# Kernel optimization log

Measured on AMD Instinct MI355X. Metric: run time of the kernel, lower is better.

Reference implementation:

```python
import jax, jax.numpy as jnp
import numpy as np

B, S, HID = 1, 2048, 2048
NH, NKV = 16, 4
HD = HID // NH  # 128


def _rope_manual(x, cos_h, sin_h):
    # x: [B, S, nh, HD]; cos_h/sin_h: [1, S, 1, HD//2]
    d = x.shape[-1]
    x_rot = x[..., : d // 2]
    x_pass = x[..., d // 2:]
    # rotate interleaved pairs inside the first half
    x_rot = jnp.stack([-x_rot[..., 1::2], x_rot[..., ::2]], axis=-1)
    x_rot = x_rot.reshape(x_rot.shape[:-2] + (d // 2,))
    return jnp.concatenate(
        [x_rot * cos_h + x_pass * sin_h, -x_rot * sin_h + x_pass * cos_h], axis=-1
    )


def setup_inputs() -> dict:
    key = jax.random.key(0)
    ks = jax.random.split(key, 7)
    bound = 1.0 / np.sqrt(HID)
    return {
        "x": jax.random.normal(ks[0], (B, S, HID), jnp.float32),
        "cos": jax.random.uniform(ks[1], (S, HD), jnp.float32),
        "sin": jax.random.uniform(ks[2], (S, HD), jnp.float32),
        "wq": jax.random.uniform(ks[3], (NH * HD, HID), jnp.float32, -bound, bound),
        "wk": jax.random.uniform(ks[4], (NKV * HD, HID), jnp.float32, -bound, bound),
        "wv": jax.random.uniform(ks[5], (NKV * HD, HID), jnp.float32, -bound, bound),
        "wo": jax.random.uniform(ks[6], (HID, HID), jnp.float32, -bound, bound),
    }


def reference(x, cos, sin, wq, wk, wv, wo):
    b, s, _ = x.shape
    q = jnp.einsum("bsh,oh->bso", x, wq).reshape(b, s, NH, HD)
    k = jnp.einsum("bsh,oh->bso", x, wk).reshape(b, s, NKV, HD)
    v = jnp.einsum("bsh,oh->bso", x, wv).reshape(b, s, NKV, HD)

    cos_h = cos[None, :, None, : HD // 2]  # [1,S,1,HD/2]
    sin_h = sin[None, :, None, : HD // 2]
    q = _rope_manual(q, cos_h, sin_h)
    k = _rope_manual(k, cos_h, sin_h)

    # [B, H, S, D]
    q = q.transpose(0, 2, 1, 3)
    k = k.transpose(0, 2, 1, 3)
    v = v.transpose(0, 2, 1, 3)
    # GQA kv repeat (repeat_interleave over head dim)
    rep = NH // NKV
    k = jnp.repeat(k, rep, axis=1)
    v = jnp.repeat(v, rep, axis=1)

    scale = 1.0 / np.sqrt(HD).astype(np.float32)
    scores = jnp.einsum("bhqd,bhkd->bhqk", q, k) * scale
    causal = jnp.tril(jnp.ones((s, s), bool))
    scores = jnp.where(causal[None, None], scores, jnp.finfo(scores.dtype).min)
    attn = jax.nn.softmax(scores, axis=-1)
    out = jnp.einsum("bhqk,bhkd->bhqd", attn, v)  # [B,H,S,D]
    out = out.transpose(0, 2, 1, 3).reshape(b, s, NH * HD)
    return jnp.einsum("bso,ho->bsh", out, wo)
```

## Files before the change

### kernel.cpp

```cpp
#include <hip/hip_runtime.h>
#include <hip/hip_bf16.h>

typedef __bf16 bf16_t;
typedef __attribute__((ext_vector_type(8))) __bf16 bf16x8;
typedef __attribute__((ext_vector_type(4))) float f32x4;

#define S_LEN 2048
#define HID 2048
#define NH 16
#define NKV 4
#define HD 128

__device__ __forceinline__ void gll16(const bf16_t* g, bf16_t* l) {
    __builtin_amdgcn_global_load_lds(
        (const __attribute__((address_space(1))) unsigned int*)g,
        (__attribute__((address_space(3))) unsigned int*)l, 16, 0, 0);
}

__device__ __forceinline__ bf16x8 cvt2x4(float4 a, float4 b) {
    bf16x8 o;
    o[0]=(bf16_t)a.x; o[1]=(bf16_t)a.y; o[2]=(bf16_t)a.z; o[3]=(bf16_t)a.w;
    o[4]=(bf16_t)b.x; o[5]=(bf16_t)b.y; o[6]=(bf16_t)b.z; o[7]=(bf16_t)b.w;
    return o;
}

__global__ __launch_bounds__(256) void cvt_f32_bf16(const float* __restrict__ in,
                                                    bf16_t* __restrict__ out, int n)
{
    int i = (blockIdx.x * 256 + threadIdx.x) * 8;
    if (i >= n) return;
    float4 a = *(const float4*)&in[i];
    float4 b = *(const float4*)&in[i + 4];
    *(bf16x8*)&out[i] = cvt2x4(a, b);
}

__global__ __launch_bounds__(256) void cvt_w3(const float* __restrict__ wq,
                                              const float* __restrict__ wk,
                                              const float* __restrict__ wv,
                                              bf16_t* __restrict__ out)
{
    int i = (blockIdx.x * 256 + threadIdx.x) * 8;
    const float* src; int off;
    if (i < 4 * 1024 * 1024)      { src = wq; off = i; }
    else if (i < 5 * 1024 * 1024) { src = wk; off = i - 4 * 1024 * 1024; }
    else                          { src = wv; off = i - 5 * 1024 * 1024; }
    float4 a = *(const float4*)&src[off];
    float4 b = *(const float4*)&src[off + 4];
    *(bf16x8*)&out[i] = cvt2x4(a, b);
}

template<int MODE, typename CT>
__global__ __launch_bounds__(256, 2) void gemm128(
    const bf16_t* __restrict__ A, const bf16_t* __restrict__ B,
    CT* __restrict__ C, bf16_t* __restrict__ CkP, bf16_t* __restrict__ CvtP,
    int N, int K)
{
    __shared__ __align__(16) bf16_t sA[128 * 64];
    __shared__ __align__(16) bf16_t sB[128 * 64];

    const int tid = threadIdx.x, lane = tid & 63, wave = tid >> 6;
    const int l16 = lane & 15, quad = lane >> 4;
    const int m0 = blockIdx.y * 128, n0 = blockIdx.x * 128;
    const int wm = (wave >> 1) * 64, wn = (wave & 1) * 64;

    const bf16_t* gA[4]; const bf16_t* gB[4];
    bf16_t* lA[4]; bf16_t* lB[4];
#pragma unroll
    for (int t = 0; t < 4; t++) {
        int p = (wave * 4 + t) * 64 + lane;
        int row = p >> 3;
        int lc = (p & 7) ^ (row & 7);
        gA[t] = A + (size_t)(m0 + row) * K + lc * 8;
        gB[t] = B + (size_t)(n0 + row) * K + lc * 8;
        lA[t] = &sA[(wave * 4 + t) * 512];
        lB[t] = &sB[(wave * 4 + t) * 512];
    }

    int offA[2][4], offB[2][4];
#pragma unroll
    for (int kc = 0; kc < 2; kc++)
#pragma unroll
        for (int i = 0; i < 4; i++) {
            int rm = wm + i * 16 + l16;
            offA[kc][i] = rm * 64 + (((kc * 4 + quad) ^ (rm & 7)) * 8);
            int rn = wn + i * 16 + l16;
            offB[kc][i] = rn * 64 + (((kc * 4 + quad) ^ (rn & 7)) * 8);
        }

    f32x4 acc[4][4] = {};

    for (int k0 = 0; k0 < K; k0 += 64) {
        __syncthreads();
#pragma unroll
        for (int t = 0; t < 4; t++) {
            gll16(gA[t], lA[t]);
            gll16(gB[t], lB[t]);
            gA[t] += 64; gB[t] += 64;
        }
        __syncthreads();

#pragma unroll
        for (int kc = 0; kc < 2; kc++) {
            bf16x8 af[4], bfv[4];
#pragma unroll
            for (int i = 0; i < 4; i++) af[i] = *(bf16x8*)&sA[offA[kc][i]];
#pragma unroll
            for (int j = 0; j < 4; j++) bfv[j] = *(bf16x8*)&sB[offB[kc][j]];
#pragma unroll
            for (int i = 0; i < 4; i++)
#pragma unroll
                for (int j = 0; j < 4; j++)
                    acc[i][j] = __builtin_amdgcn_mfma_f32_16x16x32_bf16(af[i], bfv[j], acc[i][j], 0, 0, 0);
        }
    }

#pragma unroll
    for (int i = 0; i < 4; i++) {
        int rowb = m0 + wm + i * 16 + quad * 4;
#pragma unroll
        for (int j = 0; j < 4; j++) {
            int col = n0 + wn + j * 16 + l16;
#pragma unroll
            for (int r = 0; r < 4; r++) {
                float v = acc[i][j][r];
                int row = rowb + r;
                if (MODE == 0) {
                    C[(size_t)row * N + col] = (CT)v;
                } else {
                    if (col < 2048)      C[(size_t)row * 2048 + col] = (CT)v;
                    else if (col < 2560) CkP[(size_t)row * 512 + (col - 2048)] = (bf16_t)v;
                    else                 CvtP[(size_t)(col - 2560) * S_LEN + row] = (bf16_t)v;
                }
            }
        }
    }
}

__global__ void rope_all(bf16_t* __restrict__ Qh, bf16_t* __restrict__ Kh,
                         const float* __restrict__ cosb, const float* __restrict__ sinb)
{
    int s = blockIdx.x;
    int grp = blockIdx.y;
    int sub = threadIdx.x >> 5;
    int i = threadIdx.x & 31;
    bf16_t* row = (grp < 4) ? (Qh + ((size_t)s * NH + grp * 4 + sub) * HD)
                            : (Kh + ((size_t)s * NKV + sub) * HD);
    float x0 = (float)row[2 * i];
    float x1 = (float)row[2 * i + 1];
    float p0 = (float)row[64 + 2 * i];
    float p1 = (float)row[64 + 2 * i + 1];
    float c0 = cosb[s * HD + 2 * i];
    float c1 = cosb[s * HD + 2 * i + 1];
    float n0 = sinb[s * HD + 2 * i];
    float n1 = sinb[s * HD + 2 * i + 1];
    float r0 = -x1, r1 = x0;
    row[2 * i]          = (bf16_t)(r0 * c0 + p0 * n0);
    row[2 * i + 1]      = (bf16_t)(r1 * c1 + p1 * n1);
    row[64 + 2 * i]     = (bf16_t)(-r0 * n0 + p0 * c0);
    row[64 + 2 * i + 1] = (bf16_t)(-r1 * n1 + p1 * c1);
}

__global__ __launch_bounds__(256, 2) void flash_attn3(
    const bf16_t* Q, const bf16_t* __restrict__ Kb,
    const bf16_t* __restrict__ VT, bf16_t* O, int S)
{
    __shared__ __align__(16) bf16_t sK[64 * 136];
    __shared__ __align__(16) bf16_t sVT[128 * 72];
    __shared__ __align__(16) bf16_t sP[4][16 * 72];

    const int kvh = blockIdx.y;
    const int q0  = blockIdx.x * 16;
    const int tid = threadIdx.x, lane = tid & 63, wave = tid >> 6;
    const int l16 = lane & 15, quad = lane >> 4;
    const int head = kvh * 4 + wave;
    const float scale = 0.08838834764831845f;

    bf16x8 qf[4];
#pragma unroll
    for (int c = 0; c < 4; c++)
        qf[c] = *(const bf16x8*)&Q[(size_t)(q0 + l16) * HID + head * HD + c * 32 + quad * 8];

    f32x4 oacc[8] = {};
    float lsum[4] = {};
    const int s_row = q0 + quad * 4;
    const int nkt = (blockIdx.x >> 2) + 1;

    int krow[4], kcol[4], vrow[4], vcol[4];
#pragma unroll
    for (int it = 0; it < 4; it++) {
        int c = tid + 256 * it;
        krow[it] = c >> 4; kcol[it] = (c & 15) * 8;
        vrow[it] = c >> 3; vcol[it] = (c & 7) * 8;
    }

    bf16x8 kpre[4], vpre[4];
#pragma unroll
    for (int it = 0; it < 4; it++) {
        kpre[it] = *(const bf16x8*)&Kb[(size_t)krow[it] * (NKV * HD) + kvh * HD + kcol[it]];
        vpre[it] = *(const bf16x8*)&VT[((size_t)kvh * HD + vrow[it]) * S + vcol[it]];
    }

    for (int kt = 0; kt < nkt; kt++) {
        const int t0 = kt * 64;
        __syncthreads();
#pragma unroll
        for (int it = 0; it < 4; it++) {
            *(bf16x8*)&sK[krow[it] * 136 + kcol[it]] = kpre[it];
            *(bf16x8*)&sVT[vrow[it] * 72 + vcol[it]] = vpre[it];
        }
        __syncthreads();

        if (kt + 1 < nkt) {
            const int t1 = t0 + 64;
#pragma unroll
            for (int it = 0; it < 4; it++) {
                kpre[it] = *(const bf16x8*)&Kb[(size_t)(t1 + krow[it]) * (NKV * HD) + kvh * HD + kcol[it]];
                vpre[it] = *(const bf16x8*)&VT[((size_t)kvh * HD + vrow[it]) * S + t1 + vcol[it]];
            }
        }

        f32x4 sc[4];
#pragma unroll
        for (int nt = 0; nt < 4; nt++) {
            f32x4 d = {};
#pragma unroll
            for (int c = 0; c < 4; c++) {
                bf16x8 kf = *(bf16x8*)&sK[(nt * 16 + l16) * 136 + c * 32 + quad * 8];
                d = __builtin_amdgcn_mfma_f32_16x16x32_bf16(qf[c], kf, d, 0, 0, 0);
            }
            sc[nt] = d;
        }

#pragma unroll
        for (int nt = 0; nt < 4; nt++) {
            int t = t0 + nt * 16 + l16;
#pragma unroll
            for (int r = 0; r < 4; r++) {
                float p = (t <= s_row + r) ? __expf(sc[nt][r] * scale) : 0.0f;
                lsum[r] += p;
                sP[wave][(quad * 4 + r) * 72 + nt * 16 + l16] = (bf16_t)p;
            }
        }
        bf16x8 pa[2];
#pragma unroll
        for (int kc = 0; kc < 2; kc++)
            pa[kc] = *(bf16x8*)&sP[wave][l16 * 72 + kc * 32 + quad * 8];

#pragma unroll
        for (int dt = 0; dt < 8; dt++)
#pragma unroll
            for (int kc = 0; kc < 2; kc++) {
                bf16x8 vf = *(bf16x8*)&sVT[(dt * 16 + l16) * 72 + kc * 32 + quad * 8];
                oacc[dt] = __builtin_amdgcn_mfma_f32_16x16x32_bf16(pa[kc], vf, oacc[dt], 0, 0, 0);
            }
    }

#pragma unroll
    for (int r = 0; r < 4; r++) {
        float s = lsum[r];
        for (int m = 1; m < 16; m <<= 1)
            s += __shfl_xor(s, m, 64);
        float inv = 1.0f / s;
        int srow = s_row + r;
#pragma unroll
        for (int dt = 0; dt < 8; dt++)
            O[(size_t)srow * HID + head * HD + dt * 16 + l16] = (bf16_t)(oacc[dt][r] * inv);
    }
}

extern "C" void kernel_launch(void* const* d_in, const int* in_sizes, int n_in,
                              void* d_out, int out_size, void* d_ws, size_t ws_size,
                              hipStream_t stream)
{
    const float* x    = (const float*)d_in[0];
    const float* cosb = (const float*)d_in[1];
    const float* sinb = (const float*)d_in[2];
    const float* wq   = (const float*)d_in[3];
    const float* wk   = (const float*)d_in[4];
    const float* wv   = (const float*)d_in[5];
    const float* wo   = (const float*)d_in[6];
    float* out = (float*)d_out;

    char* ws = (char*)d_ws;
    bf16_t* wb = (bf16_t*)(ws);
    bf16_t* qh = (bf16_t*)(ws + (size_t)12 * 1024 * 1024);
    bf16_t* kh = (bf16_t*)(ws + (size_t)20 * 1024 * 1024);
    bf16_t* vT = (bf16_t*)(ws + (size_t)22 * 1024 * 1024);
    bf16_t* xb = (bf16_t*)d_out;

    const int NX = S_LEN * HID;

    cvt_f32_bf16<<<NX / (256 * 8), 256, 0, stream>>>(x, xb, NX);

    cvt_w3<<<6 * 1024 * 1024 / (256 * 8), 256, 0, stream>>>(wq, wk, wv, wb);

    gemm128<1, bf16_t><<<dim3(24, 16), 256, 0, stream>>>(xb, wb, qh, kh, vT, 3072, HID);

    rope_all<<<dim3(S_LEN, 5), 128, 0, stream>>>(qh, kh, cosb, sinb);

    flash_attn3<<<dim3(S_LEN / 16, NKV), 256, 0, stream>>>(qh, kh, vT, qh, S_LEN);

    cvt_f32_bf16<<<NX / (256 * 8), 256, 0, stream>>>(wo, wb, NX);

    gemm128<0, float><<<dim3(16, 16), 256, 0, stream>>>(qh, wb, out, nullptr, nullptr, HID, HID);
}
```

Before: 260.6 us.

## Share K/V tiles across all four GQA heads and pair causal query tiles

The flash attention kernel now has each block handle all four query heads that share a KV head, with each wave owning 16 query rows. Every K/V tile loaded into shared memory is therefore reused four times. Each block processes two 64-row query tiles (qt and 31-qt) so causal work is balanced across blocks. The grid shrinks to 16x4 = 64 blocks with 4x8 accumulators per thread, which cuts parallelism to far fewer blocks than the device has CUs and raises register pressure (launch bounds drop to 1).

After: 371.9 us. 1.43x slower.

```diff
diff --git a/kernel.cpp b/kernel.cpp
--- a/kernel.cpp
+++ b/kernel.cpp
@@ -3,6 +3,7 @@
 
 typedef __bf16 bf16_t;
 typedef __attribute__((ext_vector_type(8))) __bf16 bf16x8;
+typedef __attribute__((ext_vector_type(4))) __bf16 bf16x4;
 typedef __attribute__((ext_vector_type(4))) float f32x4;
 
 #define S_LEN 2048
@@ -160,30 +161,21 @@
     row[64 + 2 * i + 1] = (bf16_t)(-r1 * n1 + p1 * c1);
 }
 
-__global__ __launch_bounds__(256, 2) void flash_attn3(
-    const bf16_t* Q, const bf16_t* __restrict__ Kb,
-    const bf16_t* __restrict__ VT, bf16_t* O, int S)
+__global__ __launch_bounds__(256, 1) void flash_attn4(
+    const bf16_t* Q,
+    const bf16_t* __restrict__ Kb,
+    const bf16_t* __restrict__ VT,
+    bf16_t* O, int S)
 {
     __shared__ __align__(16) bf16_t sK[64 * 136];
     __shared__ __align__(16) bf16_t sVT[128 * 72];
     __shared__ __align__(16) bf16_t sP[4][16 * 72];
 
     const int kvh = blockIdx.y;
-    const int q0  = blockIdx.x * 16;
+    const int h0  = kvh * 4;
     const int tid = threadIdx.x, lane = tid & 63, wave = tid >> 6;
     const int l16 = lane & 15, quad = lane >> 4;
-    const int head = kvh * 4 + wave;
     const float scale = 0.08838834764831845f;
-
-    bf16x8 qf[4];
-#pragma unroll
-    for (int c = 0; c < 4; c++)
-        qf[c] = *(const bf16x8*)&Q[(size_t)(q0 + l16) * HID + head * HD + c * 32 + quad * 8];
-
-    f32x4 oacc[8] = {};
-    float lsum[4] = {};
-    const int s_row = q0 + quad * 4;
-    const int nkt = (blockIdx.x >> 2) + 1;
 
     int krow[4], kcol[4], vrow[4], vcol[4];
 #pragma unroll
@@ -193,78 +185,98 @@
         vrow[it] = c >> 3; vcol[it] = (c & 7) * 8;
     }
 
-    bf16x8 kpre[4], vpre[4];
-#pragma unroll
-    for (int it = 0; it < 4; it++) {
-        kpre[it] = *(const bf16x8*)&Kb[(size_t)krow[it] * (NKV * HD) + kvh * HD + kcol[it]];
-        vpre[it] = *(const bf16x8*)&VT[((size_t)kvh * HD + vrow[it]) * S + vcol[it]];
-    }
-
-    for (int kt = 0; kt < nkt; kt++) {
-        const int t0 = kt * 64;
-        __syncthreads();
+    for (int phase = 0; phase < 2; phase++) {
+        const int qt  = (phase == 0) ? (31 - (int)blockIdx.x) : (int)blockIdx.x;
+        const int q0  = qt * 64;
+        const int nkt = qt + 1;
+        const int qrow = q0 + wave * 16 + l16;
+
+        bf16x8 qf[4][4];
+#pragma unroll
+        for (int h = 0; h < 4; h++)
+#pragma unroll
+            for (int c = 0; c < 4; c++)
+                qf[h][c] = *(const bf16x8*)&Q[(size_t)qrow * HID + (h0 + h) * HD + c * 32 + quad * 8];
+
+        f32x4 oacc[4][8] = {};
+        float lsum[4] = {0.f, 0.f, 0.f, 0.f};
+
+        bf16x8 kpre[4], vpre[4];
 #pragma unroll
         for (int it = 0; it < 4; it++) {
-            *(bf16x8*)&sK[krow[it] * 136 + kcol[it]] = kpre[it];
-            *(bf16x8*)&sVT[vrow[it] * 72 + vcol[it]] = vpre[it];
-        }
-        __syncthreads();
-
-        if (kt + 1 < nkt) {
-            const int t1 = t0 + 64;
+            kpre[it] = *(const bf16x8*)&Kb[(size_t)krow[it] * (NKV * HD) + kvh * HD + kcol[it]];
+            vpre[it] = *(const bf16x8*)&VT[((size_t)kvh * HD + vrow[it]) * S + vcol[it]];
+        }
+
+        for (int kt = 0; kt < nkt; kt++) {
+            const int t0 = kt * 64;
+            __syncthreads();
 #pragma unroll
             for (int it = 0; it < 4; it++) {
-                kpre[it] = *(const bf16x8*)&Kb[(size_t)(t1 + krow[it]) * (NKV * HD) + kvh * HD + kcol[it]];
-                vpre[it] = *(const bf16x8*)&VT[((size_t)kvh * HD + vrow[it]) * S + t1 + vcol[it]];
-            }
-        }
-
-        f32x4 sc[4];
-#pragma unroll
-        for (int nt = 0; nt < 4; nt++) {
-            f32x4 d = {};
-#pragma unroll
-            for (int c = 0; c < 4; c++) {
-                bf16x8 kf = *(bf16x8*)&sK[(nt * 16 + l16) * 136 + c * 32 + quad * 8];
-                d = __builtin_amdgcn_mfma_f32_16x16x32_bf16(qf[c], kf, d, 0, 0, 0);
-            }
-            sc[nt] = d;
-        }
-
-#pragma unroll
-        for (int nt = 0; nt < 4; nt++) {
-            int t = t0 + nt * 16 + l16;
+                *(bf16x8*)&sK[krow[it] * 136 + kcol[it]] = kpre[it];
+                *(bf16x8*)&sVT[vrow[it] * 72 + vcol[it]] = vpre[it];
+            }
+            __syncthreads();
+
+            if (kt + 1 < nkt) {
+                const int t1 = t0 + 64;
+#pragma unroll
+                for (int it = 0; it < 4; it++) {
+                    kpre[it] = *(const bf16x8*)&Kb[(size_t)(t1 + krow[it]) * (NKV * HD) + kvh * HD + kcol[it]];
+                    vpre[it] = *(const bf16x8*)&VT[((size_t)kvh * HD + vrow[it]) * S + t1 + vcol[it]];
+                }
+            }
+
+#pragma unroll
+            for (int h = 0; h < 4; h++) {
+#pragma unroll
+                for (int nt = 0; nt < 4; nt++) {
+                    f32x4 d = {};
+#pragma unroll
+                    for (int c = 0; c < 4; c++) {
+                        bf16x8 kf = *(bf16x8*)&sK[(nt * 16 + l16) * 136 + c * 32 + quad * 8];
+                        d = __builtin_amdgcn_mfma_f32_16x16x32_bf16(kf, qf[h][c], d, 0, 0, 0);
+                    }
+                    const int tb = t0 + nt * 16 + quad * 4;
+                    bf16x4 pk;
+#pragma unroll
+                    for (int r = 0; r < 4; r++) {
+                        float p = (tb + r <= qrow) ? __expf(d[r] * scale) : 0.0f;
+                        lsum[h] += p;
+                        pk[r] = (bf16_t)p;
+                    }
+                    *(bf16x4*)&sP[wave][l16 * 72 + nt * 16 + quad * 4] = pk;
+                }
+                bf16x8 pa[2];
+#pragma unroll
+                for (int kc = 0; kc < 2; kc++)
+                    pa[kc] = *(bf16x8*)&sP[wave][l16 * 72 + kc * 32 + quad * 8];
+
+#pragma unroll
+                for (int dt = 0; dt < 8; dt++)
+#pragma unroll
+                    for (int kc = 0; kc < 2; kc++) {
+                        bf16x8 vf = *(bf16x8*)&sVT[(dt * 16 + l16) * 72 + kc * 32 + quad * 8];
+                        oacc[h][dt] = __builtin_amdgcn_mfma_f32_16x16x32_bf16(pa[kc], vf, oacc[h][dt], 0, 0, 0);
+                    }
+            }
+        }
+
+#pragma unroll
+        for (int h = 0; h < 4; h++) {
+            float lr = lsum[h];
+            lr += __shfl_xor(lr, 16, 64);
+            lr += __shfl_xor(lr, 32, 64);
 #pragma unroll
             for (int r = 0; r < 4; r++) {
-                float p = (t <= s_row + r) ? __expf(sc[nt][r] * scale) : 0.0f;
-                lsum[r] += p;
-                sP[wave][(quad * 4 + r) * 72 + nt * 16 + l16] = (bf16_t)p;
-            }
-        }
-        bf16x8 pa[2];
-#pragma unroll
-        for (int kc = 0; kc < 2; kc++)
-            pa[kc] = *(bf16x8*)&sP[wave][l16 * 72 + kc * 32 + quad * 8];
-
-#pragma unroll
-        for (int dt = 0; dt < 8; dt++)
-#pragma unroll
-            for (int kc = 0; kc < 2; kc++) {
-                bf16x8 vf = *(bf16x8*)&sVT[(dt * 16 + l16) * 72 + kc * 32 + quad * 8];
-                oacc[dt] = __builtin_amdgcn_mfma_f32_16x16x32_bf16(pa[kc], vf, oacc[dt], 0, 0, 0);
-            }
-    }
-
-#pragma unroll
-    for (int r = 0; r < 4; r++) {
-        float s = lsum[r];
-        for (int m = 1; m < 16; m <<= 1)
-            s += __shfl_xor(s, m, 64);
-        float inv = 1.0f / s;
-        int srow = s_row + r;
-#pragma unroll
-        for (int dt = 0; dt < 8; dt++)
-            O[(size_t)srow * HID + head * HD + dt * 16 + l16] = (bf16_t)(oacc[dt][r] * inv);
+                float linv = 1.0f / __shfl(lr, quad * 4 + r, 64);
+                int srow = q0 + wave * 16 + quad * 4 + r;
+#pragma unroll
+                for (int dt = 0; dt < 8; dt++)
+                    O[(size_t)srow * HID + (h0 + h) * HD + dt * 16 + l16] =
+                        (bf16_t)(oacc[h][dt][r] * linv);
+            }
+        }
     }
 }
 
@@ -298,7 +310,7 @@
 
     rope_all<<<dim3(S_LEN, 5), 128, 0, stream>>>(qh, kh, cosb, sinb);
 
-    flash_attn3<<<dim3(S_LEN / 16, NKV), 256, 0, stream>>>(qh, kh, vT, qh, S_LEN);
+    flash_attn4<<<dim3(16, NKV), 256, 0, stream>>>(qh, kh, vT, qh, S_LEN);
 
     cvt_f32_bf16<<<NX / (256 * 8), 256, 0, stream>>>(wo, wb, NX);
 
```
